# Performance work log

Measured on AMD Instinct MI355X. Metric: run time of the kernel, lower is better.

Reference implementation:

```python
import jax, jax.numpy as jnp
import numpy as np

BN_EPS = 1e-5


def setup_inputs() -> dict:
    key = jax.random.key(0)
    k1, k2, k3, k4 = jax.random.split(key, 4)
    B, C_in, T, V = 64, 64, 300, 25
    K, C_out = 3, 64
    x = jax.random.normal(k1, (B, C_in, T, V), dtype=jnp.float32)
    # 1x1 Conv2d weight collapsed to (K*C_out, C_in); bias (K*C_out,)
    W = jax.random.normal(k2, (K * C_out, C_in), dtype=jnp.float32) * (1.0 / np.sqrt(C_in))
    b = jax.random.normal(k3, (K * C_out,), dtype=jnp.float32) * 0.02
    A = jax.random.uniform(k4, (K, V, V), dtype=jnp.float32)
    gamma = jnp.ones((C_out,), dtype=jnp.float32)
    beta = jnp.zeros((C_out,), dtype=jnp.float32)
    return {"x": x, "W": W, "b": b, "A": A, "gamma": gamma, "beta": beta}


def reference(x, W, b, A, gamma, beta):
    B, C_in, T, V = x.shape
    K = A.shape[0]
    C_out = W.shape[0] // K
    # 1x1 conv == per-pixel matmul over channels
    x_conv = jnp.einsum('bctv,oc->botv', x, W) + b[None, :, None, None]
    # split into K partitions: (B, K, C_out, T, V)
    x_conv = x_conv.reshape(B, K, C_out, T, V)
    # fused per-partition graph matmul + sum over partitions
    out = jnp.einsum('bkctv,kvw->bctw', x_conv, A)
    # BatchNorm2d (training mode: batch statistics over B, T, V)
    mean = jnp.mean(out, axis=(0, 2, 3), keepdims=True)
    var = jnp.var(out, axis=(0, 2, 3), keepdims=True)  # biased variance
    out_hat = (out - mean) * jax.lax.rsqrt(var + BN_EPS)
    return out_hat * gamma[None, :, None, None] + beta[None, :, None, None]
```

## Files before the change

### kernel.cpp

```cpp
#include <hip/hip_runtime.h>
#include <stdint.h>


#define TT 4
#define NPIX (TT * 25)
#define NT1 7
#define NBLK 4800

typedef short bf16x8 __attribute__((ext_vector_type(8)));
typedef float f32x4 __attribute__((ext_vector_type(4)));

__device__ inline short f2bf(float f) {
    union { float f; uint32_t u; } v; v.f = f;
    uint32_t u = v.u;
    u += 0x7fffu + ((u >> 16) & 1u);
    return (short)(u >> 16);
}

__global__ __launch_bounds__(256, 2) void sgc_main(
    const float* __restrict__ x, const float* __restrict__ W,
    const float* __restrict__ bias, const float* __restrict__ A,
    float* __restrict__ out, float* __restrict__ stats_part)
{
    __shared__ __align__(16) short xT[7168];
    __shared__ __align__(16) short Ylds[24576];
    __shared__ __align__(16) short Acat[3072];

    const int tid  = threadIdx.x;
    const int lane = tid & 63;
    const int wave = tid >> 6;
    const int bid  = blockIdx.x;
    const int b    = bid / 75;
    const int t0   = (bid % 75) * TT;

    bf16x8 z8 = {0,0,0,0,0,0,0,0};
    #pragma unroll
    for (int j = 0; j < 12; ++j)
        *(bf16x8*)&Ylds[(tid + 256 * j) * 8] = z8;

    {
        const size_t xbase = (size_t)b * 480000 + (size_t)t0 * 25;
        #pragma unroll
        for (int j = 0; j < 7; ++j) {
            int e4 = tid + 256 * j;
            if (e4 < 1600) {
                int ci = e4 / 25;
                int n  = (e4 % 25) * 4;
                const float4 v = *(const float4*)&x[xbase + (size_t)ci * 7500 + n];
                #pragma unroll
                for (int i = 0; i < 4; ++i) {
                    int nn = n + i;
                    int sidx = ((nn >> 4) * 2 + (ci >> 5)) * 512
                             + ((ci >> 3) & 3) * 128 + (nn & 15) * 8 + (ci & 7);
                    xT[sidx] = f2bf(((const float*)&v)[i]);
                }
            }
        }
    }

    #pragma unroll
    for (int j = 0; j < 12; ++j) {
        int s    = tid + 256 * j;
        int tile = s >> 9;
        int q    = s & 511;
        int oct  = q >> 7;
        int wl   = (q >> 3) & 15;
        int jj   = s & 7;
        int nt2  = tile / 3, kb2 = tile % 3;
        int w    = nt2 * 16 + wl;
        int kv   = kb2 * 32 + oct * 8 + jj;
        int k    = kv >> 5, v = kv & 31;
        float val = (v < 25 && w < 25) ? A[(k * 25 + v) * 25 + w] : 0.f;
        Acat[s] = f2bf(val);
    }

    bf16x8 wfrag[3][2];
    #pragma unroll
    for (int mti = 0; mti < 3; ++mti) {
        int o = (wave * 3 + mti) * 16 + (lane & 15);
        #pragma unroll
        for (int kb = 0; kb < 2; ++kb) {
            int ci0 = kb * 32 + (lane >> 4) * 8;
            const float4 f0 = *(const float4*)&W[o * 64 + ci0];
            const float4 f1 = *(const float4*)&W[o * 64 + ci0 + 4];
            bf16x8 f;
            f[0] = f2bf(f0.x); f[1] = f2bf(f0.y); f[2] = f2bf(f0.z); f[3] = f2bf(f0.w);
            f[4] = f2bf(f1.x); f[5] = f2bf(f1.y); f[6] = f2bf(f1.z); f[7] = f2bf(f1.w);
            wfrag[mti][kb] = f;
        }
    }

    float bval[3][4];
    #pragma unroll
    for (int mti = 0; mti < 3; ++mti)
        #pragma unroll
        for (int r = 0; r < 4; ++r)
            bval[mti][r] = bias[(wave * 3 + mti) * 16 + (lane >> 4) * 4 + r];

    __syncthreads();

    f32x4 acc[3][NT1];
    #pragma unroll
    for (int mti = 0; mti < 3; ++mti)
        #pragma unroll
        for (int nt = 0; nt < NT1; ++nt) {
            f32x4 zf = {0.f, 0.f, 0.f, 0.f};
            acc[mti][nt] = zf;
        }

    #pragma unroll
    for (int nt = 0; nt < NT1; ++nt) {
        bf16x8 xb0 = *(const bf16x8*)&xT[((nt * 2 + 0) * 64 + lane) * 8];
        bf16x8 xb1 = *(const bf16x8*)&xT[((nt * 2 + 1) * 64 + lane) * 8];
        #pragma unroll
        for (int mti = 0; mti < 3; ++mti) {
            acc[mti][nt] = __builtin_amdgcn_mfma_f32_16x16x32_bf16(
                wfrag[mti][0], xb0, acc[mti][nt], 0, 0, 0);
            acc[mti][nt] = __builtin_amdgcn_mfma_f32_16x16x32_bf16(
                wfrag[mti][1], xb1, acc[mti][nt], 0, 0, 0);
        }
    }

    #pragma unroll
    for (int nt = 0; nt < NT1; ++nt) {
        int n = nt * 16 + (lane & 15);
        if (n < NPIX) {
            int t = n / 25, v = n % 25;
            #pragma unroll
            for (int mti = 0; mti < 3; ++mti) {
                int obase = (wave * 3 + mti) * 16 + (lane >> 4) * 4;
                #pragma unroll
                for (int r = 0; r < 4; ++r) {
                    int o = obase + r;
                    int k = o >> 6, c = o & 63;
                    int kv = k * 32 + v;
                    float val = acc[mti][nt][r] + bval[mti][r];
                    int sidx = ((t * 4 + (c >> 4)) * 3 + k) * 512
                             + ((kv >> 3) & 3) * 128 + (c & 15) * 8 + (kv & 7);
                    Ylds[sidx] = f2bf(val);
                }
            }
        }
    }
    __syncthreads();

    bf16x8 bfrag2[2][3];
    #pragma unroll
    for (int nt2 = 0; nt2 < 2; ++nt2)
        #pragma unroll
        for (int kb2 = 0; kb2 < 3; ++kb2)
            bfrag2[nt2][kb2] = *(const bf16x8*)&Acat[((nt2 * 3 + kb2) * 64 + lane) * 8];

    float ssum[4] = {0.f, 0.f, 0.f, 0.f};
    float ssq[4]  = {0.f, 0.f, 0.f, 0.f};
    const int c0 = wave * 16 + (lane >> 4) * 4;

    #pragma unroll
    for (int t = 0; t < TT; ++t) {
        bf16x8 a2[3];
        #pragma unroll
        for (int kb2 = 0; kb2 < 3; ++kb2)
            a2[kb2] = *(const bf16x8*)&Ylds[(((t * 4 + wave) * 3 + kb2) * 64 + lane) * 8];

        f32x4 acc2[2];
        #pragma unroll
        for (int nt2 = 0; nt2 < 2; ++nt2) {
            f32x4 zf = {0.f, 0.f, 0.f, 0.f};
            acc2[nt2] = zf;
            #pragma unroll
            for (int kb2 = 0; kb2 < 3; ++kb2)
                acc2[nt2] = __builtin_amdgcn_mfma_f32_16x16x32_bf16(
                    a2[kb2], bfrag2[nt2][kb2], acc2[nt2], 0, 0, 0);
        }

        #pragma unroll
        for (int nt2 = 0; nt2 < 2; ++nt2) {
            int w = nt2 * 16 + (lane & 15);
            bool valid = (w < 25);
            #pragma unroll
            for (int r = 0; r < 4; ++r) {
                float val = acc2[nt2][r];
                if (valid) {
                    out[(size_t)((b * 64 + c0 + r) * 300 + t0 + t) * 25 + w] = val;
                    ssum[r] += val;
                    ssq[r]  += val * val;
                }
            }
        }
    }

    #pragma unroll
    for (int r = 0; r < 4; ++r) {
        float s = ssum[r], q = ssq[r];
        #pragma unroll
        for (int d = 1; d < 16; d <<= 1) {
            s += __shfl_xor(s, d);
            q += __shfl_xor(q, d);
        }
        if ((lane & 15) == 0) {
            int c = c0 + r;
            int slot = bid & 63;
            atomicAdd(&stats_part[slot * 128 + c], s);
            atomicAdd(&stats_part[slot * 128 + 64 + c], q);
        }
    }
}

__global__ void sgc_finalize(const float* __restrict__ stats_part,
                             const float* __restrict__ gamma,
                             const float* __restrict__ beta,
                             float* __restrict__ scaleshift)
{
    int c = threadIdx.x;
    float s = 0.f, q = 0.f;
    #pragma unroll 8
    for (int slot = 0; slot < 64; ++slot) {
        s += stats_part[slot * 128 + c];
        q += stats_part[slot * 128 + 64 + c];
    }
    const float invN = 1.f / 480000.f;
    float mean = s * invN;
    float var  = q * invN - mean * mean;
    float rstd = rsqrtf(var + 1e-5f);
    float sc = rstd * gamma[c];
    scaleshift[c]      = sc;
    scaleshift[64 + c] = beta[c] - mean * sc;
}

__global__ __launch_bounds__(256) void sgc_norm(float* __restrict__ out,
                                                const float* __restrict__ scaleshift)
{
    const int total4 = 30720000 / 4;
    int stride = gridDim.x * 256;
    for (int i = blockIdx.x * 256 + threadIdx.x; i < total4; i += stride) {
        int c = (i / 1875) & 63;
        float sc = scaleshift[c], sh = scaleshift[64 + c];
        float4 v = *((float4*)out + i);
        v.x = v.x * sc + sh;
        v.y = v.y * sc + sh;
        v.z = v.z * sc + sh;
        v.w = v.w * sc + sh;
        *((float4*)out + i) = v;
    }
}

extern "C" void kernel_launch(void* const* d_in, const int* in_sizes, int n_in,
                              void* d_out, int out_size, void* d_ws, size_t ws_size,
                              hipStream_t stream)
{
    const float* x     = (const float*)d_in[0];
    const float* W     = (const float*)d_in[1];
    const float* bias  = (const float*)d_in[2];
    const float* A     = (const float*)d_in[3];
    const float* gamma = (const float*)d_in[4];
    const float* beta  = (const float*)d_in[5];
    float* out = (float*)d_out;

    float* stats      = (float*)d_ws;
    float* scaleshift = stats + 64 * 128;

    hipMemsetAsync(stats, 0, 64 * 128 * sizeof(float), stream);
    sgc_main<<<NBLK, 256, 0, stream>>>(x, W, bias, A, out, stats);
    sgc_finalize<<<1, 64, 0, stream>>>(stats, gamma, beta, scaleshift);
    sgc_norm<<<4096, 256, 0, stream>>>(out, scaleshift);
}
```

Baseline: 345.5 us.

## Store pre-norm output as bf16 intermediate and shrink LDS to raise occupancy

The main kernel now writes the graph-conv result to a bf16 workspace buffer, padded to 32 along w, and the normalization pass reads bf16 and writes fp32 once. This avoids the fp32 write-then-read-modify-write of the full output. It also merges the three LDS arrays into one reused buffer, raises launch bounds to 3 blocks/SM, and swaps MFMA operand order so stores are vectorized. It also builds the A fragments directly in registers and uses packed bf16 conversion. The bf16 intermediate adds rounding error before normalization, and the fast path depends on having enough workspace.

```diff
diff --git a/kernel.cpp b/kernel.cpp
--- a/kernel.cpp
+++ b/kernel.cpp
@@ -1,208 +1,197 @@
 #include <hip/hip_runtime.h>
+#include <hip/hip_bf16.h>
 #include <stdint.h>
 
 
-#define TT 4
-#define NPIX (TT * 25)
-#define NT1 7
 #define NBLK 4800
 
 typedef short bf16x8 __attribute__((ext_vector_type(8)));
+typedef short short4v __attribute__((ext_vector_type(4)));
 typedef float f32x4 __attribute__((ext_vector_type(4)));
 
-__device__ inline short f2bf(float f) {
-    union { float f; uint32_t u; } v; v.f = f;
-    uint32_t u = v.u;
-    u += 0x7fffu + ((u >> 16) & 1u);
-    return (short)(u >> 16);
-}
-
-__global__ __launch_bounds__(256, 2) void sgc_main(
+struct __attribute__((packed, aligned(4))) F4U { float x, y, z, w; };
+
+static __device__ inline uint32_t pk2(float a, float b) {
+    __hip_bfloat162 h = __float22bfloat162_rn(float2{a, b});
+    union { __hip_bfloat162 h; uint32_t u; } cv; cv.h = h; return cv.u;
+}
+
+template<bool BF16OUT>
+__global__ __launch_bounds__(256, 3) void sgc_main(
     const float* __restrict__ x, const float* __restrict__ W,
     const float* __restrict__ bias, const float* __restrict__ A,
-    float* __restrict__ out, float* __restrict__ stats_part)
-{
-    __shared__ __align__(16) short xT[7168];
-    __shared__ __align__(16) short Ylds[24576];
-    __shared__ __align__(16) short Acat[3072];
+    float* __restrict__ outf, uint16_t* __restrict__ yi,
+    float* __restrict__ stats_part)
+{
+    __shared__ __align__(16) short buf[24576];
 
     const int tid  = threadIdx.x;
     const int lane = tid & 63;
     const int wave = tid >> 6;
     const int bid  = blockIdx.x;
     const int b    = bid / 75;
-    const int t0   = (bid % 75) * TT;
-
-    bf16x8 z8 = {0,0,0,0,0,0,0,0};
-    #pragma unroll
-    for (int j = 0; j < 12; ++j)
-        *(bf16x8*)&Ylds[(tid + 256 * j) * 8] = z8;
+    const int t0   = (bid % 75) * 4;
+
+    bf16x8 wfrag[3][2];
+    float bval[3];
+    #pragma unroll
+    for (int oti = 0; oti < 3; ++oti) {
+        int o = (wave * 3 + oti) * 16 + (lane & 15);
+        bval[oti] = bias[o];
+        #pragma unroll
+        for (int kb = 0; kb < 2; ++kb) {
+            const float4 f0 = *(const float4*)&W[o * 64 + kb * 32 + (lane >> 4) * 8];
+            const float4 f1 = *(const float4*)&W[o * 64 + kb * 32 + (lane >> 4) * 8 + 4];
+            union { bf16x8 v; uint32_t u[4]; } p;
+            p.u[0] = pk2(f0.x, f0.y); p.u[1] = pk2(f0.z, f0.w);
+            p.u[2] = pk2(f1.x, f1.y); p.u[3] = pk2(f1.z, f1.w);
+            wfrag[oti][kb] = p.v;
+        }
+    }
 
     {
         const size_t xbase = (size_t)b * 480000 + (size_t)t0 * 25;
         #pragma unroll
-        for (int j = 0; j < 7; ++j) {
-            int e4 = tid + 256 * j;
-            if (e4 < 1600) {
-                int ci = e4 / 25;
-                int n  = (e4 % 25) * 4;
-                const float4 v = *(const float4*)&x[xbase + (size_t)ci * 7500 + n];
+        for (int it = 0; it < 2; ++it) {
+            int slot = tid + 256 * it;
+            if (slot < 400) {
+                int oc = slot / 50;
+                int m  = slot - oc * 50;
+                int n  = 2 * m;
+                const float* xp = x + xbase + (size_t)oc * 60000 + n;
+                float2 v[8];
                 #pragma unroll
-                for (int i = 0; i < 4; ++i) {
-                    int nn = n + i;
-                    int sidx = ((nn >> 4) * 2 + (ci >> 5)) * 512
-                             + ((ci >> 3) & 3) * 128 + (nn & 15) * 8 + (ci & 7);
-                    xT[sidx] = f2bf(((const float*)&v)[i]);
+                for (int jj = 0; jj < 8; ++jj)
+                    v[jj] = *(const float2*)(xp + 7500 * jj);
+                union { bf16x8 vv; uint32_t u[4]; } c0, c1;
+                #pragma unroll
+                for (int q = 0; q < 4; ++q) {
+                    c0.u[q] = pk2(v[2*q].x, v[2*q+1].x);
+                    c1.u[q] = pk2(v[2*q].y, v[2*q+1].y);
+                }
+                int kb = oc >> 2, oct = oc & 3;
+                int t = n / 25;  int p0 = t * 28 + (n - t * 25);
+                int n1 = n + 1;  int t1 = n1 / 25;
+                int p1 = t1 * 28 + (n1 - t1 * 25);
+                *(bf16x8*)&buf[(((p0 >> 4) * 2 + kb) * 64 + oct * 16 + (p0 & 15)) * 8] = c0.vv;
+                *(bf16x8*)&buf[(((p1 >> 4) * 2 + kb) * 64 + oct * 16 + (p1 & 15)) * 8] = c1.vv;
+            }
+        }
+    }
+    __syncthreads();
+
+    f32x4 acc[3][7];
+    #pragma unroll
+    for (int oti = 0; oti < 3; ++oti)
+        #pragma unroll
+        for (int nt = 0; nt < 7; ++nt) {
+            f32x4 z = {0.f, 0.f, 0.f, 0.f};
+            acc[oti][nt] = z;
+        }
+    #pragma unroll
+    for (int nt = 0; nt < 7; ++nt) {
+        bf16x8 xa0 = *(const bf16x8*)&buf[((nt * 2 + 0) * 64 + lane) * 8];
+        bf16x8 xa1 = *(const bf16x8*)&buf[((nt * 2 + 1) * 64 + lane) * 8];
+        #pragma unroll
+        for (int oti = 0; oti < 3; ++oti) {
+            acc[oti][nt] = __builtin_amdgcn_mfma_f32_16x16x32_bf16(
+                xa0, wfrag[oti][0], acc[oti][nt], 0, 0, 0);
+            acc[oti][nt] = __builtin_amdgcn_mfma_f32_16x16x32_bf16(
+                xa1, wfrag[oti][1], acc[oti][nt], 0, 0, 0);
+        }
+    }
+    __syncthreads();
+
+    bf16x8 bfrag2[2][3];
+    #pragma unroll
+    for (int mt = 0; mt < 2; ++mt) {
+        int w = mt * 16 + (lane & 15);
+        #pragma unroll
+        for (int kb2 = 0; kb2 < 3; ++kb2) {
+            union { bf16x8 vv; uint32_t u[4]; } p;
+            #pragma unroll
+            for (int q = 0; q < 4; ++q) {
+                int v0 = (lane >> 4) * 8 + 2 * q;
+                float a0 = (w < 25 && v0     < 25) ? A[(kb2 * 25 + v0    ) * 25 + w] : 0.f;
+                float a1 = (w < 25 && v0 + 1 < 25) ? A[(kb2 * 25 + v0 + 1) * 25 + w] : 0.f;
+                p.u[q] = pk2(a0, a1);
+            }
+            bfrag2[mt][kb2] = p.vv;
+        }
+    }
+
+    #pragma unroll
+    for (int oti = 0; oti < 3; ++oti) {
+        int o = (wave * 3 + oti) * 16 + (lane & 15);
+        int k = o >> 6, c = o & 63;
+        float bv = bval[oti];
+        int cbase = (c >> 4) * 3 + k;
+        int cl = c & 15;
+        #pragma unroll
+        for (int nt = 0; nt < 7; ++nt) {
+            int p0 = nt * 16 + (lane >> 4) * 4;
+            int t  = p0 / 28;
+            int v0 = p0 - t * 28;
+            f32x4 a = acc[oti][nt];
+            float e0 = a[0] + bv;
+            float e1 = (v0 == 24) ? 0.f : a[1] + bv;
+            float e2 = (v0 == 24) ? 0.f : a[2] + bv;
+            float e3 = (v0 == 24) ? 0.f : a[3] + bv;
+            union { short4v s; uint32_t u[2]; } pk;
+            pk.u[0] = pk2(e0, e1); pk.u[1] = pk2(e2, e3);
+            int addr = ((t * 12 + cbase) * 64 + (v0 >> 3) * 16 + cl) * 8 + (v0 & 7);
+            *(short4v*)&buf[addr] = pk.s;
+        }
+    }
+    #pragma unroll
+    for (int zz = 0; zz < 3; ++zz) {
+        int z = tid + 256 * zz;
+        int cl = z & 15, rest = z >> 4;
+        short4v zero4 = {0, 0, 0, 0};
+        *(short4v*)&buf[(rest * 64 + 48 + cl) * 8 + 4] = zero4;
+    }
+    __syncthreads();
+
+    float ssum = 0.f, ssq = 0.f;
+    const int c = wave * 16 + (lane & 15);
+    #pragma unroll
+    for (int t = 0; t < 4; ++t) {
+        bf16x8 yb[3];
+        #pragma unroll
+        for (int kb2 = 0; kb2 < 3; ++kb2)
+            yb[kb2] = *(const bf16x8*)&buf[(((t * 4 + wave) * 3 + kb2) * 64 + lane) * 8];
+        #pragma unroll
+        for (int mt = 0; mt < 2; ++mt) {
+            f32x4 a2 = {0.f, 0.f, 0.f, 0.f};
+            #pragma unroll
+            for (int kb2 = 0; kb2 < 3; ++kb2)
+                a2 = __builtin_amdgcn_mfma_f32_16x16x32_bf16(
+                    bfrag2[mt][kb2], yb[kb2], a2, 0, 0, 0);
+            int w0 = mt * 16 + (lane >> 4) * 4;
+            #pragma unroll
+            for (int r = 0; r < 4; ++r)
+                if (w0 + r < 25) { ssum += a2[r]; ssq += a2[r] * a2[r]; }
+            if (BF16OUT) {
+                union { short4v s; uint32_t u[2]; } pk;
+                pk.u[0] = pk2(a2[0], a2[1]); pk.u[1] = pk2(a2[2], a2[3]);
+                *(short4v*)&yi[(size_t)(b * 300 + t0 + t) * 2048 + c * 32 + w0] = pk.s;
+            } else {
+                size_t ob = (size_t)(b * 64 + c) * 7500 + (size_t)(t0 + t) * 25 + w0;
+                if (w0 < 24) {
+                    F4U s = {a2[0], a2[1], a2[2], a2[3]};
+                    *(F4U*)&outf[ob] = s;
+                } else if (w0 == 24) {
+                    outf[ob] = a2[0];
                 }
             }
         }
     }
-
-    #pragma unroll
-    for (int j = 0; j < 12; ++j) {
-        int s    = tid + 256 * j;
-        int tile = s >> 9;
-        int q    = s & 511;
-        int oct  = q >> 7;
-        int wl   = (q >> 3) & 15;
-        int jj   = s & 7;
-        int nt2  = tile / 3, kb2 = tile % 3;
-        int w    = nt2 * 16 + wl;
-        int kv   = kb2 * 32 + oct * 8 + jj;
-        int k    = kv >> 5, v = kv & 31;
-        float val = (v < 25 && w < 25) ? A[(k * 25 + v) * 25 + w] : 0.f;
-        Acat[s] = f2bf(val);
-    }
-
-    bf16x8 wfrag[3][2];
-    #pragma unroll
-    for (int mti = 0; mti < 3; ++mti) {
-        int o = (wave * 3 + mti) * 16 + (lane & 15);
-        #pragma unroll
-        for (int kb = 0; kb < 2; ++kb) {
-            int ci0 = kb * 32 + (lane >> 4) * 8;
-            const float4 f0 = *(const float4*)&W[o * 64 + ci0];
-            const float4 f1 = *(const float4*)&W[o * 64 + ci0 + 4];
-            bf16x8 f;
-            f[0] = f2bf(f0.x); f[1] = f2bf(f0.y); f[2] = f2bf(f0.z); f[3] = f2bf(f0.w);
-            f[4] = f2bf(f1.x); f[5] = f2bf(f1.y); f[6] = f2bf(f1.z); f[7] = f2bf(f1.w);
-            wfrag[mti][kb] = f;
-        }
-    }
-
-    float bval[3][4];
-    #pragma unroll
-    for (int mti = 0; mti < 3; ++mti)
-        #pragma unroll
-        for (int r = 0; r < 4; ++r)
-            bval[mti][r] = bias[(wave * 3 + mti) * 16 + (lane >> 4) * 4 + r];
-
-    __syncthreads();
-
-    f32x4 acc[3][NT1];
-    #pragma unroll
-    for (int mti = 0; mti < 3; ++mti)
-        #pragma unroll
-        for (int nt = 0; nt < NT1; ++nt) {
-            f32x4 zf = {0.f, 0.f, 0.f, 0.f};
-            acc[mti][nt] = zf;
-        }
-
-    #pragma unroll
-    for (int nt = 0; nt < NT1; ++nt) {
-        bf16x8 xb0 = *(const bf16x8*)&xT[((nt * 2 + 0) * 64 + lane) * 8];
-        bf16x8 xb1 = *(const bf16x8*)&xT[((nt * 2 + 1) * 64 + lane) * 8];
-        #pragma unroll
-        for (int mti = 0; mti < 3; ++mti) {
-            acc[mti][nt] = __builtin_amdgcn_mfma_f32_16x16x32_bf16(
-                wfrag[mti][0], xb0, acc[mti][nt], 0, 0, 0);
-            acc[mti][nt] = __builtin_amdgcn_mfma_f32_16x16x32_bf16(
-                wfrag[mti][1], xb1, acc[mti][nt], 0, 0, 0);
-        }
-    }
-
-    #pragma unroll
-    for (int nt = 0; nt < NT1; ++nt) {
-        int n = nt * 16 + (lane & 15);
-        if (n < NPIX) {
-            int t = n / 25, v = n % 25;
-            #pragma unroll
-            for (int mti = 0; mti < 3; ++mti) {
-                int obase = (wave * 3 + mti) * 16 + (lane >> 4) * 4;
-                #pragma unroll
-                for (int r = 0; r < 4; ++r) {
-                    int o = obase + r;
-                    int k = o >> 6, c = o & 63;
-                    int kv = k * 32 + v;
-                    float val = acc[mti][nt][r] + bval[mti][r];
-                    int sidx = ((t * 4 + (c >> 4)) * 3 + k) * 512
-                             + ((kv >> 3) & 3) * 128 + (c & 15) * 8 + (kv & 7);
-                    Ylds[sidx] = f2bf(val);
-                }
-            }
-        }
-    }
-    __syncthreads();
-
-    bf16x8 bfrag2[2][3];
-    #pragma unroll
-    for (int nt2 = 0; nt2 < 2; ++nt2)
-        #pragma unroll
-        for (int kb2 = 0; kb2 < 3; ++kb2)
-            bfrag2[nt2][kb2] = *(const bf16x8*)&Acat[((nt2 * 3 + kb2) * 64 + lane) * 8];
-
-    float ssum[4] = {0.f, 0.f, 0.f, 0.f};
-    float ssq[4]  = {0.f, 0.f, 0.f, 0.f};
-    const int c0 = wave * 16 + (lane >> 4) * 4;
-
-    #pragma unroll
-    for (int t = 0; t < TT; ++t) {
-        bf16x8 a2[3];
-        #pragma unroll
-        for (int kb2 = 0; kb2 < 3; ++kb2)
-            a2[kb2] = *(const bf16x8*)&Ylds[(((t * 4 + wave) * 3 + kb2) * 64 + lane) * 8];
-
-        f32x4 acc2[2];
-        #pragma unroll
-        for (int nt2 = 0; nt2 < 2; ++nt2) {
-            f32x4 zf = {0.f, 0.f, 0.f, 0.f};
-            acc2[nt2] = zf;
-            #pragma unroll
-            for (int kb2 = 0; kb2 < 3; ++kb2)
-                acc2[nt2] = __builtin_amdgcn_mfma_f32_16x16x32_bf16(
-                    a2[kb2], bfrag2[nt2][kb2], acc2[nt2], 0, 0, 0);
-        }
-
-        #pragma unroll
-        for (int nt2 = 0; nt2 < 2; ++nt2) {
-            int w = nt2 * 16 + (lane & 15);
-            bool valid = (w < 25);
-            #pragma unroll
-            for (int r = 0; r < 4; ++r) {
-                float val = acc2[nt2][r];
-                if (valid) {
-                    out[(size_t)((b * 64 + c0 + r) * 300 + t0 + t) * 25 + w] = val;
-                    ssum[r] += val;
-                    ssq[r]  += val * val;
-                }
-            }
-        }
-    }
-
-    #pragma unroll
-    for (int r = 0; r < 4; ++r) {
-        float s = ssum[r], q = ssq[r];
-        #pragma unroll
-        for (int d = 1; d < 16; d <<= 1) {
-            s += __shfl_xor(s, d);
-            q += __shfl_xor(q, d);
-        }
-        if ((lane & 15) == 0) {
-            int c = c0 + r;
-            int slot = bid & 63;
-            atomicAdd(&stats_part[slot * 128 + c], s);
-            atomicAdd(&stats_part[slot * 128 + 64 + c], q);
-        }
+    ssum += __shfl_xor(ssum, 16); ssum += __shfl_xor(ssum, 32);
+    ssq  += __shfl_xor(ssq, 16);  ssq  += __shfl_xor(ssq, 32);
+    if (lane < 16) {
+        int slot = bid & 63;
+        atomicAdd(&stats_part[slot * 128 + c], ssum);
+        atomicAdd(&stats_part[slot * 128 + 64 + c], ssq);
     }
 }
 
@@ -227,14 +216,47 @@
     scaleshift[64 + c] = beta[c] - mean * sc;
 }
 
-__global__ __launch_bounds__(256) void sgc_norm(float* __restrict__ out,
-                                                const float* __restrict__ scaleshift)
+__global__ __launch_bounds__(256) void sgc_norm_bf(
+    const uint16_t* __restrict__ yi, const float* __restrict__ ss,
+    float* __restrict__ out)
+{
+    const int nch = 64 * 300 * 2048 / 8;
+    int stride = gridDim.x * 256;
+    for (int i = blockIdx.x * 256 + threadIdx.x; i < nch; i += stride) {
+        int flat = i << 3;
+        int w0 = flat & 31;
+        int c  = (flat >> 5) & 63;
+        int row = (int)((unsigned)flat >> 11);
+        int b = row / 300, t = row - b * 300;
+        float sc = ss[c], sh = ss[64 + c];
+        bf16x8 y = *(const bf16x8*)&yi[(size_t)flat];
+        float f[8];
+        #pragma unroll
+        for (int j = 0; j < 8; ++j) {
+            union { uint32_t u; float fv; } cv;
+            cv.u = ((uint32_t)(uint16_t)y[j]) << 16;
+            f[j] = cv.fv * sc + sh;
+        }
+        size_t ob = (size_t)(b * 64 + c) * 7500 + (size_t)t * 25 + w0;
+        if (w0 < 24) {
+            F4U s0 = {f[0], f[1], f[2], f[3]};
+            F4U s1 = {f[4], f[5], f[6], f[7]};
+            *(F4U*)&out[ob] = s0;
+            *(F4U*)&out[ob + 4] = s1;
+        } else {
+            out[ob] = f[0];
+        }
+    }
+}
+
+__global__ __launch_bounds__(256) void sgc_norm_fp(float* __restrict__ out,
+                                                   const float* __restrict__ ss)
 {
     const int total4 = 30720000 / 4;
     int stride = gridDim.x * 256;
     for (int i = blockIdx.x * 256 + threadIdx.x; i < total4; i += stride) {
         int c = (i / 1875) & 63;
-        float sc = scaleshift[c], sh = scaleshift[64 + c];
+        float sc = ss[c], sh = ss[64 + c];
         float4 v = *((float4*)out + i);
         v.x = v.x * sc + sh;
         v.y = v.y * sc + sh;
@@ -258,9 +280,17 @@
 
     float* stats      = (float*)d_ws;
     float* scaleshift = stats + 64 * 128;
+    uint16_t* yi      = (uint16_t*)((char*)d_ws + 40960);
+    const size_t need = (size_t)64 * 300 * 2048 * 2 + 40960;
 
     hipMemsetAsync(stats, 0, 64 * 128 * sizeof(float), stream);
-    sgc_main<<<NBLK, 256, 0, stream>>>(x, W, bias, A, out, stats);
-    sgc_finalize<<<1, 64, 0, stream>>>(stats, gamma, beta, scaleshift);
-    sgc_norm<<<4096, 256, 0, stream>>>(out, scaleshift);
-}
+    if (ws_size >= need) {
+        sgc_main<true><<<NBLK, 256, 0, stream>>>(x, W, bias, A, out, yi, stats);
+        sgc_finalize<<<1, 64, 0, stream>>>(stats, gamma, beta, scaleshift);
+        sgc_norm_bf<<<4096, 256, 0, stream>>>(yi, scaleshift, out);
+    } else {
+        sgc_main<false><<<NBLK, 256, 0, stream>>>(x, W, bias, A, out, nullptr, stats);
+        sgc_finalize<<<1, 64, 0, stream>>>(stats, gamma, beta, scaleshift);
+        sgc_norm_fp<<<4096, 256, 0, stream>>>(out, scaleshift);
+    }
+}
```

Measured after the change: 370.7 us. 7.3% more time.
